# Optimization experiments

Measured on AMD Instinct MI355X. Metric: run time of the kernel, lower is better.

Reference implementation:

```python
import jax, jax.numpy as jnp
import numpy as np

N_NODES = 100000
N_EDGES = 1600000
D_FEAT = 64
NUM_LAYERS = 3


def setup_inputs() -> dict:
    key = jax.random.key(0)
    k1, k2, k3, k4 = jax.random.split(key, 4)
    X = jax.random.normal(k1, (N_NODES, D_FEAT), dtype=jnp.float32)
    src = jax.random.randint(k2, (N_EDGES,), 0, N_NODES, dtype=jnp.int32)
    dst = jax.random.randint(k3, (N_EDGES,), 0, N_NODES, dtype=jnp.int32)
    ew = jax.random.uniform(k4, (N_EDGES,), dtype=jnp.float32)
    return {"X": X, "src": src, "dst": dst, "ew": ew}


def _spmm(X, src, dst, ew):
    # gather source features, scale by edge weight, scatter-sum into dst
    msgs = X[src] * ew[:, None]  # [E, d]
    return jax.ops.segment_sum(msgs, dst, num_segments=N_NODES)


def reference(X, src, dst, ew):
    # LightGCNConv with stack_layers=True: average of layer-0..num_layers embeddings
    X_list = [X]
    h = X
    for _ in range(NUM_LAYERS):
        h = _spmm(h, src, dst, ew)
        X_list.append(h)
    return jnp.mean(jnp.stack(X_list, axis=1), axis=1)  # [N, d]
```

## Files before the change

### kernel.cpp

```cpp
#include <hip/hip_runtime.h>
#include <hip/hip_fp16.h>

#define N_NODES 100000
#define D_FEAT  64
#define N_EDGES 1600000
#define NPB     128
#define NBUCK   ((N_NODES + NPB - 1) / NPB)
#define CAP     3072
#define CVT_BLOCKS  256
#define CVT_THREADS 1024
#define CHUNK   (N_EDGES / CVT_BLOCKS)
#define PULL_BLOCKS 2048
#define GRP     4
#define GCAP    512
#define GPAD    (GCAP + 64)
#define SORT_CAP CAP

__global__ void init_bcur(int* __restrict__ bcur) {
    int t = threadIdx.x;
    if (t < NBUCK) bcur[t] = 0;
}

__global__ __launch_bounds__(CVT_THREADS) void cvt_part(const float* __restrict__ X,
                                                        __half* __restrict__ Xh,
                                                        const int* __restrict__ src,
                                                        const int* __restrict__ dst,
                                                        const float* __restrict__ ew,
                                                        int* __restrict__ bcur,
                                                        int2* __restrict__ bedges) {
    __shared__ int h[NBUCK];
    const int t = threadIdx.x;
    for (int i = t; i < NBUCK; i += CVT_THREADS) h[i] = 0;

    const int n4 = N_NODES * D_FEAT / 4;
    for (int i = blockIdx.x * CVT_THREADS + t; i < n4; i += CVT_BLOCKS * CVT_THREADS) {
        float4 v = ((const float4*)X)[i];
        ((__half2*)Xh)[2 * i]     = __floats2half2_rn(v.x, v.y);
        ((__half2*)Xh)[2 * i + 1] = __floats2half2_rn(v.z, v.w);
    }
    __syncthreads();

    const int beg = blockIdx.x * CHUNK, end = beg + CHUNK;
    for (int i = beg + t; i < end; i += CVT_THREADS)
        atomicAdd(&h[dst[i] >> 7], 1);
    __syncthreads();

    for (int i = t; i < NBUCK; i += CVT_THREADS) {
        int c = h[i];
        h[i] = c ? atomicAdd(&bcur[i], c) : 0;
    }
    __syncthreads();

    for (int i = beg + t; i < end; i += CVT_THREADS) {
        int d = dst[i];
        int b = d >> 7;
        int p = atomicAdd(&h[b], 1);
        if (p < CAP) {
            int2 e;
            e.x = src[i] | ((d & (NPB - 1)) << 17);
            e.y = __float_as_int(ew[i]);
            bedges[(size_t)b * CAP + p] = e;
        }
    }
}

__global__ void scan_bcnt(const int* __restrict__ bcnt, int* __restrict__ bptr,
                          int* __restrict__ row_ptr) {
    __shared__ int tmp[1024];
    const int t = threadIdx.x;
    int v = (t < NBUCK) ? bcnt[t] : 0;
    if (v > CAP) v = CAP;
    tmp[t] = v;
    __syncthreads();
    for (int off = 1; off < 1024; off <<= 1) {
        int u = (t >= off) ? tmp[t - off] : 0;
        __syncthreads();
        tmp[t] += u;
        __syncthreads();
    }
    if (t < NBUCK) bptr[t] = tmp[t] - v;
    if (t == NBUCK - 1) {
        bptr[NBUCK] = tmp[t];
        row_ptr[N_NODES] = tmp[t];
    }
}

__global__ __launch_bounds__(256) void sort_bucket(const int2* __restrict__ bedges,
                                                   const int* __restrict__ bcnt,
                                                   const int* __restrict__ bptr,
                                                   int2* __restrict__ sedges,
                                                   int* __restrict__ row_ptr) {
    __shared__ int cnt[NPB], sc[NPB], cur[NPB];
    __shared__ int2 buf[SORT_CAP];
    const int b = blockIdx.x, t = threadIdx.x;
    const int ibeg = b * CAP;
    const int obeg = bptr[b];
    int n = bcnt[b];
    if (n > CAP) n = CAP;

    if (t < NPB) cnt[t] = 0;
    __syncthreads();
    for (int i = t; i < n; i += 256) {
        int2 e = bedges[ibeg + i];
        buf[i] = e;
        atomicAdd(&cnt[e.x >> 17], 1);
    }
    __syncthreads();

    if (t < NPB) sc[t] = cnt[t];
    __syncthreads();
    for (int off = 1; off < NPB; off <<= 1) {
        int v = (t >= off && t < NPB) ? sc[t - off] : 0;
        __syncthreads();
        if (t < NPB) sc[t] += v;
        __syncthreads();
    }
    if (t < NPB) {
        cur[t] = sc[t] - cnt[t];
        int node = b * NPB + t;
        if (node < N_NODES) row_ptr[node] = obeg + sc[t] - cnt[t];
    }
    __syncthreads();

    for (int i = t; i < n; i += 256) {
        int2 e = buf[i];
        int p = atomicAdd(&cur[e.x >> 17], 1);
        sedges[obeg + p] = make_int2(e.x & 0x1FFFF, e.y);
    }
}

template <int MODE>
__global__ __launch_bounds__(256) void spmm_pull(const __half* __restrict__ hprev,
                                                 const int* __restrict__ row_ptr,
                                                 const int2* __restrict__ edges,
                                                 __half* __restrict__ hout,
                                                 float* __restrict__ out,
                                                 const float* __restrict__ X,
                                                 const __half* __restrict__ h1,
                                                 const __half* __restrict__ h2) {
    __shared__ int2 ebuf[GPAD];
    __shared__ int  rp[GRP + 1];
    __shared__ int  pbase[GRP + 1];
    const int t    = threadIdx.x;
    const int wid  = t >> 6;
    const int lane = t & 63;
    const int half = lane >> 5;
    const int sub  = lane & 31;
    const int ngroups = (N_NODES + GRP - 1) / GRP;

    for (int g = blockIdx.x; g < ngroups; g += gridDim.x) {
        const int n0 = g * GRP;
        if (t <= GRP) {
            int nn = n0 + t;
            rp[t] = row_ptr[nn < N_NODES ? nn : N_NODES];
        }
        __syncthreads();
        const int B = rp[0], E = rp[GRP];
        const int cnt = E - B;

        if (cnt <= GCAP) {
            if (t == 0) {
                int o = 0;
                #pragma unroll
                for (int i = 0; i < GRP; ++i) {
                    pbase[i] = o;
                    o += (rp[i + 1] - rp[i] + 15) & ~15;
                }
                pbase[GRP] = o;
            }
            __syncthreads();
            for (int i = t; i < cnt; i += 256) {
                int p = B + i;
                int nd = (p >= rp[1]) + (p >= rp[2]) + (p >= rp[3]);
                ebuf[pbase[nd] + (p - rp[nd])] = edges[p];
            }
            if (t < GRP * 15) {
                int i = t / 15;
                int slot = pbase[i] + (rp[i + 1] - rp[i]) + (t % 15);
                if (slot < pbase[i + 1]) ebuf[slot] = make_int2(0, 0);
            }
            __syncthreads();
            int node = n0 + wid;
            if (node < N_NODES) {
                const int d  = rp[wid + 1] - rp[wid];
                const int pb = pbase[wid] + half;
                const int nb = (d + 15) >> 4;
                float ax = 0.0f, ay = 0.0f;
                for (int bi = 0; bi < nb; ++bi) {
                    const int base = pb + bi * 16;
                    unsigned tv[8]; float w[8];
                    #pragma unroll
                    for (int k = 0; k < 8; ++k) {
                        int2 e = ebuf[base + 2 * k];
                        w[k]  = __int_as_float(e.y);
                        tv[k] = *(const unsigned*)(hprev + (((size_t)e.x << 6) | (2 * sub)));
                    }
                    #pragma unroll
                    for (int k = 0; k < 8; ++k) {
                        float2 f = __half22float2(*(__half2*)&tv[k]);
                        ax += f.x * w[k];
                        ay += f.y * w[k];
                    }
                }
                ax += __shfl_xor(ax, 32);
                ay += __shfl_xor(ay, 32);
                if (half == 0) {
                    size_t bo = (size_t)node * 32 + sub;
                    if (MODE == 2) {
                        float2 x  = ((const float2*)X)[bo];
                        float2 f1 = __half22float2(((const __half2*)h1)[bo]);
                        float2 f2 = __half22float2(((const __half2*)h2)[bo]);
                        ((float2*)out)[bo] = make_float2((x.x + f1.x + f2.x + ax) * 0.25f,
                                                         (x.y + f1.y + f2.y + ay) * 0.25f);
                    } else {
                        ((__half2*)hout)[bo] = __floats2half2_rn(ax, ay);
                    }
                }
            }
            __syncthreads();
        } else {
            int node = n0 + wid;
            if (node < N_NODES) {
                int beg = __builtin_amdgcn_readfirstlane(row_ptr[node]);
                int end = __builtin_amdgcn_readfirstlane(row_ptr[node + 1]);
                float ax = 0.0f, ay = 0.0f;
                for (int j = beg; j < end; j += 16) {
                    unsigned tv[8]; float w[8];
                    #pragma unroll
                    for (int k = 0; k < 8; ++k) {
                        int i0 = j + 2 * k, i1 = i0 + 1;
                        int2 e0 = edges[(i0 < end) ? i0 : beg];
                        int2 e1 = edges[(i1 < end) ? i1 : beg];
                        int s = half ? e1.x : e0.x;
                        float w0 = (i0 < end) ? __int_as_float(e0.y) : 0.0f;
                        float w1 = (i1 < end) ? __int_as_float(e1.y) : 0.0f;
                        w[k] = half ? w1 : w0;
                        tv[k] = *(const unsigned*)(hprev + (((size_t)s << 6) | (2 * sub)));
                    }
                    #pragma unroll
                    for (int k = 0; k < 8; ++k) {
                        float2 f = __half22float2(*(__half2*)&tv[k]);
                        ax += f.x * w[k];
                        ay += f.y * w[k];
                    }
                }
                ax += __shfl_xor(ax, 32);
                ay += __shfl_xor(ay, 32);
                if (half == 0) {
                    size_t bo = (size_t)node * 32 + sub;
                    if (MODE == 2) {
                        float2 x  = ((const float2*)X)[bo];
                        float2 f1 = __half22float2(((const __half2*)h1)[bo]);
                        float2 f2 = __half22float2(((const __half2*)h2)[bo]);
                        ((float2*)out)[bo] = make_float2((x.x + f1.x + f2.x + ax) * 0.25f,
                                                         (x.y + f1.y + f2.y + ay) * 0.25f);
                    } else {
                        ((__half2*)hout)[bo] = __floats2half2_rn(ax, ay);
                    }
                }
            }
            __syncthreads();
        }
    }
}

extern "C" void kernel_launch(void* const* d_in, const int* in_sizes, int n_in,
                              void* d_out, int out_size, void* d_ws, size_t ws_size,
                              hipStream_t stream) {
    const float* X   = (const float*)d_in[0];
    const int*   src = (const int*)  d_in[1];
    const int*   dst = (const int*)  d_in[2];
    const float* ew  = (const float*)d_in[3];
    float* out = (float*)d_out;

    const size_t feat = (size_t)N_NODES * D_FEAT;

    char* p = (char*)d_ws;
    __half* hA     = (__half*)p; p += feat * sizeof(__half);
    __half* hB     = (__half*)p; p += feat * sizeof(__half);
    __half* Xh     = (__half*)p; p += feat * sizeof(__half);
    int2*  sedges  = (int2*)p;   p += (size_t)N_EDGES * sizeof(int2);
    int*   row_ptr = (int*)p;    p += ((size_t)N_NODES + 1) * 4;
    int*   bcur    = (int*)p;    p += (size_t)NBUCK * 4;
    int*   bptr    = (int*)p;    p += ((size_t)NBUCK + 1) * 4;

    int2* bedges = (int2*)hA;

    init_bcur <<<1, 1024, 0, stream>>>(bcur);
    cvt_part  <<<CVT_BLOCKS, CVT_THREADS, 0, stream>>>(X, Xh, src, dst, ew, bcur, bedges);
    scan_bcnt <<<1, 1024, 0, stream>>>(bcur, bptr, row_ptr);
    sort_bucket<<<NBUCK, 256, 0, stream>>>(bedges, bcur, bptr, sedges, row_ptr);

    spmm_pull<0><<<PULL_BLOCKS, 256, 0, stream>>>(Xh, row_ptr, sedges, hA, out, X, hA, hB);
    spmm_pull<1><<<PULL_BLOCKS, 256, 0, stream>>>(hA, row_ptr, sedges, hB, out, X, hA, hB);
    spmm_pull<2><<<PULL_BLOCKS, 256, 0, stream>>>(hB, row_ptr, sedges, (__half*)nullptr, out, X, hA, hB);
}
```

Measured before the change: 245.9 us.

## Replace bucketed two-pass CSR build with per-node counting sort via global atomics

Builds the CSR directly from a per-node histogram of destination indices, using a global atomic per edge, followed by a two-level prefix scan and an atomic-cursor scatter of (src, weight) pairs. This replaces the old scheme, which bucketed edges into 128-node buckets through shared-memory atomics and then sorted each bucket in LDS. The goal is to drop the intermediate bucket buffer pass and the fixed per-bucket capacity clamp. The cost is 1.6M contended global atomics in both the histogram and the scatter, plus random global writes and nondeterministic edge order within each row.

Measured after the change: 396.6 us. 1.61x slower.

```diff
diff --git a/kernel.cpp b/kernel.cpp
--- a/kernel.cpp
+++ b/kernel.cpp
@@ -6,70 +6,57 @@
 #define N_EDGES 1600000
 #define NPB     128
 #define NBUCK   ((N_NODES + NPB - 1) / NPB)
-#define CAP     3072
 #define CVT_BLOCKS  256
 #define CVT_THREADS 1024
-#define CHUNK   (N_EDGES / CVT_BLOCKS)
 #define PULL_BLOCKS 2048
 #define GRP     4
 #define GCAP    512
 #define GPAD    (GCAP + 64)
-#define SORT_CAP CAP
-
-__global__ void init_bcur(int* __restrict__ bcur) {
-    int t = threadIdx.x;
-    if (t < NBUCK) bcur[t] = 0;
-}
-
-__global__ __launch_bounds__(CVT_THREADS) void cvt_part(const float* __restrict__ X,
+
+__global__ __launch_bounds__(256) void zero_cnt(int* __restrict__ ncnt) {
+    int i = blockIdx.x * 256 + threadIdx.x;
+    if (i < N_NODES) ncnt[i] = 0;
+}
+
+__global__ __launch_bounds__(CVT_THREADS) void cvt_hist(const float* __restrict__ X,
                                                         __half* __restrict__ Xh,
-                                                        const int* __restrict__ src,
                                                         const int* __restrict__ dst,
-                                                        const float* __restrict__ ew,
-                                                        int* __restrict__ bcur,
-                                                        int2* __restrict__ bedges) {
-    __shared__ int h[NBUCK];
-    const int t = threadIdx.x;
-    for (int i = t; i < NBUCK; i += CVT_THREADS) h[i] = 0;
-
+                                                        int* __restrict__ ncnt) {
+    const int t = blockIdx.x * CVT_THREADS + threadIdx.x;
+    const int stride = CVT_BLOCKS * CVT_THREADS;
     const int n4 = N_NODES * D_FEAT / 4;
-    for (int i = blockIdx.x * CVT_THREADS + t; i < n4; i += CVT_BLOCKS * CVT_THREADS) {
+    for (int i = t; i < n4; i += stride) {
         float4 v = ((const float4*)X)[i];
         ((__half2*)Xh)[2 * i]     = __floats2half2_rn(v.x, v.y);
         ((__half2*)Xh)[2 * i + 1] = __floats2half2_rn(v.z, v.w);
     }
+    for (int i = t; i < N_EDGES; i += stride)
+        atomicAdd(&ncnt[dst[i]], 1);
+}
+
+__global__ __launch_bounds__(NPB) void scan128(int* __restrict__ ncnt,
+                                               int* __restrict__ btot) {
+    __shared__ int tmp[NPB];
+    const int t = threadIdx.x;
+    const int idx = blockIdx.x * NPB + t;
+    int v = (idx < N_NODES) ? ncnt[idx] : 0;
+    tmp[t] = v;
     __syncthreads();
-
-    const int beg = blockIdx.x * CHUNK, end = beg + CHUNK;
-    for (int i = beg + t; i < end; i += CVT_THREADS)
-        atomicAdd(&h[dst[i] >> 7], 1);
-    __syncthreads();
-
-    for (int i = t; i < NBUCK; i += CVT_THREADS) {
-        int c = h[i];
-        h[i] = c ? atomicAdd(&bcur[i], c) : 0;
-    }
-    __syncthreads();
-
-    for (int i = beg + t; i < end; i += CVT_THREADS) {
-        int d = dst[i];
-        int b = d >> 7;
-        int p = atomicAdd(&h[b], 1);
-        if (p < CAP) {
-            int2 e;
-            e.x = src[i] | ((d & (NPB - 1)) << 17);
-            e.y = __float_as_int(ew[i]);
-            bedges[(size_t)b * CAP + p] = e;
-        }
-    }
-}
-
-__global__ void scan_bcnt(const int* __restrict__ bcnt, int* __restrict__ bptr,
-                          int* __restrict__ row_ptr) {
+    for (int off = 1; off < NPB; off <<= 1) {
+        int u = (t >= off) ? tmp[t - off] : 0;
+        __syncthreads();
+        tmp[t] += u;
+        __syncthreads();
+    }
+    if (idx < N_NODES) ncnt[idx] = tmp[t] - v;
+    if (t == NPB - 1) btot[blockIdx.x] = tmp[t];
+}
+
+__global__ void scan_tot(const int* __restrict__ btot, int* __restrict__ bbase,
+                         int* __restrict__ row_ptr) {
     __shared__ int tmp[1024];
     const int t = threadIdx.x;
-    int v = (t < NBUCK) ? bcnt[t] : 0;
-    if (v > CAP) v = CAP;
+    int v = (t < NBUCK) ? btot[t] : 0;
     tmp[t] = v;
     __syncthreads();
     for (int off = 1; off < 1024; off <<= 1) {
@@ -78,54 +65,36 @@
         tmp[t] += u;
         __syncthreads();
     }
-    if (t < NBUCK) bptr[t] = tmp[t] - v;
+    if (t < NBUCK) bbase[t] = tmp[t] - v;
     if (t == NBUCK - 1) {
-        bptr[NBUCK] = tmp[t];
+        bbase[NBUCK] = tmp[t];
         row_ptr[N_NODES] = tmp[t];
     }
 }
 
-__global__ __launch_bounds__(256) void sort_bucket(const int2* __restrict__ bedges,
-                                                   const int* __restrict__ bcnt,
-                                                   const int* __restrict__ bptr,
-                                                   int2* __restrict__ sedges,
-                                                   int* __restrict__ row_ptr) {
-    __shared__ int cnt[NPB], sc[NPB], cur[NPB];
-    __shared__ int2 buf[SORT_CAP];
-    const int b = blockIdx.x, t = threadIdx.x;
-    const int ibeg = b * CAP;
-    const int obeg = bptr[b];
-    int n = bcnt[b];
-    if (n > CAP) n = CAP;
-
-    if (t < NPB) cnt[t] = 0;
-    __syncthreads();
-    for (int i = t; i < n; i += 256) {
-        int2 e = bedges[ibeg + i];
-        buf[i] = e;
-        atomicAdd(&cnt[e.x >> 17], 1);
-    }
-    __syncthreads();
-
-    if (t < NPB) sc[t] = cnt[t];
-    __syncthreads();
-    for (int off = 1; off < NPB; off <<= 1) {
-        int v = (t >= off && t < NPB) ? sc[t - off] : 0;
-        __syncthreads();
-        if (t < NPB) sc[t] += v;
-        __syncthreads();
-    }
-    if (t < NPB) {
-        cur[t] = sc[t] - cnt[t];
-        int node = b * NPB + t;
-        if (node < N_NODES) row_ptr[node] = obeg + sc[t] - cnt[t];
-    }
-    __syncthreads();
-
-    for (int i = t; i < n; i += 256) {
-        int2 e = buf[i];
-        int p = atomicAdd(&cur[e.x >> 17], 1);
-        sedges[obeg + p] = make_int2(e.x & 0x1FFFF, e.y);
+__global__ __launch_bounds__(256) void finalize(const int* __restrict__ ncnt,
+                                                const int* __restrict__ bbase,
+                                                int* __restrict__ row_ptr,
+                                                int* __restrict__ cur) {
+    int i = blockIdx.x * 256 + threadIdx.x;
+    if (i < N_NODES) {
+        int r = ncnt[i] + bbase[i >> 7];
+        row_ptr[i] = r;
+        cur[i] = r;
+    }
+}
+
+__global__ __launch_bounds__(256) void scatter(const int* __restrict__ src,
+                                               const int* __restrict__ dst,
+                                               const float* __restrict__ ew,
+                                               int* __restrict__ cur,
+                                               int2* __restrict__ sedges) {
+    const int t = blockIdx.x * 256 + threadIdx.x;
+    const int stride = gridDim.x * 256;
+    for (int i = t; i < N_EDGES; i += stride) {
+        int d = dst[i];
+        int p = atomicAdd(&cur[d], 1);
+        sedges[p] = make_int2(src[i], __float_as_int(ew[i]));
     }
 }
 
@@ -281,15 +250,19 @@
     __half* Xh     = (__half*)p; p += feat * sizeof(__half);
     int2*  sedges  = (int2*)p;   p += (size_t)N_EDGES * sizeof(int2);
     int*   row_ptr = (int*)p;    p += ((size_t)N_NODES + 1) * 4;
-    int*   bcur    = (int*)p;    p += (size_t)NBUCK * 4;
-    int*   bptr    = (int*)p;    p += ((size_t)NBUCK + 1) * 4;
-
-    int2* bedges = (int2*)hA;
-
-    init_bcur <<<1, 1024, 0, stream>>>(bcur);
-    cvt_part  <<<CVT_BLOCKS, CVT_THREADS, 0, stream>>>(X, Xh, src, dst, ew, bcur, bedges);
-    scan_bcnt <<<1, 1024, 0, stream>>>(bcur, bptr, row_ptr);
-    sort_bucket<<<NBUCK, 256, 0, stream>>>(bedges, bcur, bptr, sedges, row_ptr);
+    int*   ncnt    = (int*)p;    p += (size_t)N_NODES * 4;
+    int*   cur     = (int*)p;    p += (size_t)N_NODES * 4;
+    int*   btot    = (int*)p;    p += (size_t)NBUCK * 4;
+    int*   bbase   = (int*)p;    p += ((size_t)NBUCK + 1) * 4;
+
+    const int nb_nodes = (N_NODES + 255) / 256;
+
+    zero_cnt <<<nb_nodes, 256, 0, stream>>>(ncnt);
+    cvt_hist <<<CVT_BLOCKS, CVT_THREADS, 0, stream>>>(X, Xh, dst, ncnt);
+    scan128  <<<NBUCK, NPB, 0, stream>>>(ncnt, btot);
+    scan_tot <<<1, 1024, 0, stream>>>(btot, bbase, row_ptr);
+    finalize <<<nb_nodes, 256, 0, stream>>>(ncnt, bbase, row_ptr, cur);
+    scatter  <<<2048, 256, 0, stream>>>(src, dst, ew, cur, sedges);
 
     spmm_pull<0><<<PULL_BLOCKS, 256, 0, stream>>>(Xh, row_ptr, sedges, hA, out, X, hA, hB);
     spmm_pull<1><<<PULL_BLOCKS, 256, 0, stream>>>(hA, row_ptr, sedges, hB, out, X, hA, hB);
```

## Make SpMM pull wave-independent, staging each node's edges in per-wave LDS

Applied to the files above, without the earlier changes.

Replaces the block-level group of four nodes, which shared a padded LDS edge buffer and used several __syncthreads per group, with a per-wavefront loop where each wave owns a node. It stages up to 64 edges into its own LDS slice and falls back to direct global edge loads for higher-degree nodes. This removes block-wide barriers and the serial prefix computation by thread 0, so waves no longer stall on the slowest node in their group. It relies on intra-wave ordering of the LDS write and read without an explicit barrier.

Result: faster. 229.6 us (-6.6%).

```diff
diff --git a/kernel.cpp b/kernel.cpp
--- a/kernel.cpp
+++ b/kernel.cpp
@@ -11,9 +11,7 @@
 #define CVT_THREADS 1024
 #define CHUNK   (N_EDGES / CVT_BLOCKS)
 #define PULL_BLOCKS 2048
-#define GRP     4
-#define GCAP    512
-#define GPAD    (GCAP + 64)
+#define WCAP    64
 #define SORT_CAP CAP
 
 __global__ void init_bcur(int* __restrict__ bcur) {
@@ -138,128 +136,94 @@
                                                  const float* __restrict__ X,
                                                  const __half* __restrict__ h1,
                                                  const __half* __restrict__ h2) {
-    __shared__ int2 ebuf[GPAD];
-    __shared__ int  rp[GRP + 1];
-    __shared__ int  pbase[GRP + 1];
+    __shared__ int2 ebuf[4][WCAP];
     const int t    = threadIdx.x;
     const int wid  = t >> 6;
     const int lane = t & 63;
     const int half = lane >> 5;
     const int sub  = lane & 31;
-    const int ngroups = (N_NODES + GRP - 1) / GRP;
-
-    for (int g = blockIdx.x; g < ngroups; g += gridDim.x) {
-        const int n0 = g * GRP;
-        if (t <= GRP) {
-            int nn = n0 + t;
-            rp[t] = row_ptr[nn < N_NODES ? nn : N_NODES];
-        }
-        __syncthreads();
-        const int B = rp[0], E = rp[GRP];
-        const int cnt = E - B;
-
-        if (cnt <= GCAP) {
-            if (t == 0) {
-                int o = 0;
-                #pragma unroll
-                for (int i = 0; i < GRP; ++i) {
-                    pbase[i] = o;
-                    o += (rp[i + 1] - rp[i] + 15) & ~15;
-                }
-                pbase[GRP] = o;
-            }
-            __syncthreads();
-            for (int i = t; i < cnt; i += 256) {
-                int p = B + i;
-                int nd = (p >= rp[1]) + (p >= rp[2]) + (p >= rp[3]);
-                ebuf[pbase[nd] + (p - rp[nd])] = edges[p];
-            }
-            if (t < GRP * 15) {
-                int i = t / 15;
-                int slot = pbase[i] + (rp[i + 1] - rp[i]) + (t % 15);
-                if (slot < pbase[i + 1]) ebuf[slot] = make_int2(0, 0);
-            }
-            __syncthreads();
-            int node = n0 + wid;
-            if (node < N_NODES) {
-                const int d  = rp[wid + 1] - rp[wid];
-                const int pb = pbase[wid] + half;
-                const int nb = (d + 15) >> 4;
-                float ax = 0.0f, ay = 0.0f;
-                for (int bi = 0; bi < nb; ++bi) {
-                    const int base = pb + bi * 16;
-                    unsigned tv[8]; float w[8];
-                    #pragma unroll
-                    for (int k = 0; k < 8; ++k) {
-                        int2 e = ebuf[base + 2 * k];
-                        w[k]  = __int_as_float(e.y);
-                        tv[k] = *(const unsigned*)(hprev + (((size_t)e.x << 6) | (2 * sub)));
-                    }
-                    #pragma unroll
-                    for (int k = 0; k < 8; ++k) {
-                        float2 f = __half22float2(*(__half2*)&tv[k]);
-                        ax += f.x * w[k];
-                        ay += f.y * w[k];
-                    }
-                }
-                ax += __shfl_xor(ax, 32);
-                ay += __shfl_xor(ay, 32);
-                if (half == 0) {
-                    size_t bo = (size_t)node * 32 + sub;
-                    if (MODE == 2) {
-                        float2 x  = ((const float2*)X)[bo];
-                        float2 f1 = __half22float2(((const __half2*)h1)[bo]);
-                        float2 f2 = __half22float2(((const __half2*)h2)[bo]);
-                        ((float2*)out)[bo] = make_float2((x.x + f1.x + f2.x + ax) * 0.25f,
-                                                         (x.y + f1.y + f2.y + ay) * 0.25f);
-                    } else {
-                        ((__half2*)hout)[bo] = __floats2half2_rn(ax, ay);
-                    }
-                }
-            }
-            __syncthreads();
+    const int gw     = blockIdx.x * 4 + wid;
+    const int nwaves = gridDim.x * 4;
+
+    for (int node = gw; node < N_NODES; node += nwaves) {
+        int2 bp = *(const int2*)&row_ptr[node];
+        const int beg = bp.x, end = bp.y;
+        const int d = end - beg;
+
+        if (d <= WCAP) {
+            const int dp = (d + 15) & ~15;
+            if (lane < dp) {
+                int2 e = (lane < d) ? edges[beg + lane] : make_int2(0, 0);
+                ebuf[wid][lane] = e;
+            }
+            float ax = 0.0f, ay = 0.0f;
+            const int nb = dp >> 4;
+            for (int bi = 0; bi < nb; ++bi) {
+                const int base = bi * 16 + half;
+                unsigned tv[8]; float w[8];
+                #pragma unroll
+                for (int k = 0; k < 8; ++k) {
+                    int2 e = ebuf[wid][base + 2 * k];
+                    w[k]  = __int_as_float(e.y);
+                    tv[k] = *(const unsigned*)(hprev + (((size_t)e.x << 6) | (2 * sub)));
+                }
+                #pragma unroll
+                for (int k = 0; k < 8; ++k) {
+                    float2 f = __half22float2(*(__half2*)&tv[k]);
+                    ax += f.x * w[k];
+                    ay += f.y * w[k];
+                }
+            }
+            ax += __shfl_xor(ax, 32);
+            ay += __shfl_xor(ay, 32);
+            if (half == 0) {
+                size_t bo = (size_t)node * 32 + sub;
+                if (MODE == 2) {
+                    float2 x  = ((const float2*)X)[bo];
+                    float2 f1 = __half22float2(((const __half2*)h1)[bo]);
+                    float2 f2 = __half22float2(((const __half2*)h2)[bo]);
+                    ((float2*)out)[bo] = make_float2((x.x + f1.x + f2.x + ax) * 0.25f,
+                                                     (x.y + f1.y + f2.y + ay) * 0.25f);
+                } else {
+                    ((__half2*)hout)[bo] = __floats2half2_rn(ax, ay);
+                }
+            }
         } else {
-            int node = n0 + wid;
-            if (node < N_NODES) {
-                int beg = __builtin_amdgcn_readfirstlane(row_ptr[node]);
-                int end = __builtin_amdgcn_readfirstlane(row_ptr[node + 1]);
-                float ax = 0.0f, ay = 0.0f;
-                for (int j = beg; j < end; j += 16) {
-                    unsigned tv[8]; float w[8];
-                    #pragma unroll
-                    for (int k = 0; k < 8; ++k) {
-                        int i0 = j + 2 * k, i1 = i0 + 1;
-                        int2 e0 = edges[(i0 < end) ? i0 : beg];
-                        int2 e1 = edges[(i1 < end) ? i1 : beg];
-                        int s = half ? e1.x : e0.x;
-                        float w0 = (i0 < end) ? __int_as_float(e0.y) : 0.0f;
-                        float w1 = (i1 < end) ? __int_as_float(e1.y) : 0.0f;
-                        w[k] = half ? w1 : w0;
-                        tv[k] = *(const unsigned*)(hprev + (((size_t)s << 6) | (2 * sub)));
-                    }
-                    #pragma unroll
-                    for (int k = 0; k < 8; ++k) {
-                        float2 f = __half22float2(*(__half2*)&tv[k]);
-                        ax += f.x * w[k];
-                        ay += f.y * w[k];
-                    }
-                }
-                ax += __shfl_xor(ax, 32);
-                ay += __shfl_xor(ay, 32);
-                if (half == 0) {
-                    size_t bo = (size_t)node * 32 + sub;
-                    if (MODE == 2) {
-                        float2 x  = ((const float2*)X)[bo];
-                        float2 f1 = __half22float2(((const __half2*)h1)[bo]);
-                        float2 f2 = __half22float2(((const __half2*)h2)[bo]);
-                        ((float2*)out)[bo] = make_float2((x.x + f1.x + f2.x + ax) * 0.25f,
-                                                         (x.y + f1.y + f2.y + ay) * 0.25f);
-                    } else {
-                        ((__half2*)hout)[bo] = __floats2half2_rn(ax, ay);
-                    }
-                }
-            }
-            __syncthreads();
+            float ax = 0.0f, ay = 0.0f;
+            for (int j = beg; j < end; j += 16) {
+                unsigned tv[8]; float w[8];
+                #pragma unroll
+                for (int k = 0; k < 8; ++k) {
+                    int i0 = j + 2 * k, i1 = i0 + 1;
+                    int2 e0 = edges[(i0 < end) ? i0 : beg];
+                    int2 e1 = edges[(i1 < end) ? i1 : beg];
+                    int s = half ? e1.x : e0.x;
+                    float w0 = (i0 < end) ? __int_as_float(e0.y) : 0.0f;
+                    float w1 = (i1 < end) ? __int_as_float(e1.y) : 0.0f;
+                    w[k] = half ? w1 : w0;
+                    tv[k] = *(const unsigned*)(hprev + (((size_t)s << 6) | (2 * sub)));
+                }
+                #pragma unroll
+                for (int k = 0; k < 8; ++k) {
+                    float2 f = __half22float2(*(__half2*)&tv[k]);
+                    ax += f.x * w[k];
+                    ay += f.y * w[k];
+                }
+            }
+            ax += __shfl_xor(ax, 32);
+            ay += __shfl_xor(ay, 32);
+            if (half == 0) {
+                size_t bo = (size_t)node * 32 + sub;
+                if (MODE == 2) {
+                    float2 x  = ((const float2*)X)[bo];
+                    float2 f1 = __half22float2(((const __half2*)h1)[bo]);
+                    float2 f2 = __half22float2(((const __half2*)h2)[bo]);
+                    ((float2*)out)[bo] = make_float2((x.x + f1.x + f2.x + ax) * 0.25f,
+                                                     (x.y + f1.y + f2.y + ay) * 0.25f);
+                } else {
+                    ((__half2*)hout)[bo] = __floats2half2_rn(ax, ay);
+                }
+            }
         }
     }
 }
```
